# Kernel optimization log

Hardware: AMD Instinct MI355X
Metric: run time of the kernel (lower is better)

The kernel has to match this reference:

```python
import jax, jax.numpy as jnp
import numpy as np
import math

B, T, D = 4, 4096, 512
LN_EPS = 1e-5


def setup_inputs() -> dict:
    key = jax.random.key(0)
    ks = jax.random.split(key, 12)
    stdv = 1.0 / math.sqrt(D)
    lin = 1.0 / math.sqrt(D)  # torch Linear default init bound
    return {
        "query": jax.random.normal(ks[0], (B, T, D), jnp.float32),
        "value": jax.random.normal(ks[1], (B, T, D), jnp.float32),
        "query_vector": jax.random.uniform(ks[2], (D,), jnp.float32, -stdv, stdv),
        "key_vector": jax.random.uniform(ks[3], (D,), jnp.float32, -stdv, stdv),
        "value_vector": jax.random.uniform(ks[4], (D,), jnp.float32, -stdv, stdv),
        "Wq": jax.random.uniform(ks[5], (D, D), jnp.float32, -lin, lin),
        "bq": jax.random.uniform(ks[6], (D,), jnp.float32, -lin, lin),
        "ln_gamma": jnp.ones((D,), jnp.float32),
        "ln_beta": jnp.zeros((D,), jnp.float32),
        "Ws": jax.random.uniform(ks[7], (D, D), jnp.float32, -lin, lin),
        "bs": jax.random.uniform(ks[8], (D,), jnp.float32, -lin, lin),
        "Wt": jax.random.uniform(ks[9], (D, D), jnp.float32, -lin, lin),
        "bt": jax.random.uniform(ks[10], (D,), jnp.float32, -lin, lin),
    }


def reference(query, value, query_vector, key_vector, value_vector,
              Wq, bq, ln_gamma, ln_beta, Ws, bs, Wt, bt):
    d = query.shape[-1]
    # query linear + layernorm
    q = query @ Wq.T + bq
    mu = jnp.mean(q, axis=-1, keepdims=True)
    var = jnp.var(q, axis=-1, keepdims=True)
    q = (q - mu) * jax.lax.rsqrt(var + LN_EPS) * ln_gamma + ln_beta
    # gated Q/K/V preprocessing
    q = q * jax.nn.sigmoid(query_vector)
    k = value * jax.nn.sigmoid(key_vector)
    vv = jax.nn.sigmoid(value_vector)              # [D]
    v_sigm = jax.nn.sigmoid(vv @ Ws.T + bs)        # [D] (infer=False path)
    v_tanh = jnp.tanh(vv @ Wt.T + bt)              # [D]
    v = value * (v_sigm * v_tanh)
    # causal full attention (explicit, as in original)
    w = jnp.einsum('btd,bsd->bts', q, k) / jnp.sqrt(jnp.float32(d))
    tmask = jnp.tril(jnp.ones((q.shape[1], q.shape[1]), bool))
    w = jnp.where(tmask[None, :, :], w, -jnp.inf)
    w = jax.nn.softmax(w, axis=-1)
    return jnp.einsum('bts,bsd->btd', w, v)
```

## Files before the change

### kernel.cpp

```cpp
#include <hip/hip_runtime.h>
#include <cstdint>

typedef __bf16 bf16x8 __attribute__((ext_vector_type(8)));
typedef float f32x4 __attribute__((ext_vector_type(4)));

#define DIM 512
#define TSEQ 4096

__device__ __forceinline__ ushort f2bf(float x) {
  uint32_t u = __float_as_uint(x);
  u += 0x7fffu + ((u >> 16) & 1u);
  return (ushort)(u >> 16);
}
__device__ __forceinline__ float bf2f(ushort u) {
  return __uint_as_float(((uint32_t)u) << 16);
}

__global__ __launch_bounds__(512)
void gates_kernel(const float* __restrict__ qv, const float* __restrict__ kv,
                  const float* __restrict__ vvec,
                  const float* __restrict__ Ws, const float* __restrict__ bs,
                  const float* __restrict__ Wt, const float* __restrict__ bt,
                  const float* __restrict__ gamma, const float* __restrict__ beta,
                  float* __restrict__ gk, float* __restrict__ gv,
                  float* __restrict__ gb1, float* __restrict__ gb2) {
  __shared__ float vv[DIM];
  const int t = threadIdx.x;
  const int lane = t & 63, w = t >> 6;
  vv[t] = 1.f / (1.f + __expf(-vvec[t]));
  if (blockIdx.x == 0) {
    const float SC = 0.044194173824159216f;
    float gqv = 1.f / (1.f + __expf(-qv[t]));
    gk[t] = 1.f / (1.f + __expf(-kv[t]));
    gb1[t] = gamma[t] * gqv * SC;
    gb2[t] = beta[t] * gqv * SC;
  }
  __syncthreads();
  const int d = blockIdx.x * 8 + w;
  const float* wsr = Ws + (size_t)d * DIM + lane * 8;
  const float* wtr = Wt + (size_t)d * DIM + lane * 8;
  float4 v0 = *(const float4*)(&vv[lane * 8]);
  float4 v1 = *(const float4*)(&vv[lane * 8 + 4]);
  float4 s0 = *(const float4*)wsr, s1 = *(const float4*)(wsr + 4);
  float4 t0 = *(const float4*)wtr, t1 = *(const float4*)(wtr + 4);
  float as = v0.x*s0.x + v0.y*s0.y + v0.z*s0.z + v0.w*s0.w
           + v1.x*s1.x + v1.y*s1.y + v1.z*s1.z + v1.w*s1.w;
  float at = v0.x*t0.x + v0.y*t0.y + v0.z*t0.z + v0.w*t0.w
           + v1.x*t1.x + v1.y*t1.y + v1.z*t1.z + v1.w*t1.w;
  #pragma unroll
  for (int off = 1; off < 64; off <<= 1) {
    as += __shfl_xor(as, off, 64);
    at += __shfl_xor(at, off, 64);
  }
  if (lane == 0) {
    float sg = 1.f / (1.f + __expf(-(as + bs[d])));
    float th = tanhf(at + bt[d]);
    gv[d] = sg * th;
  }
}

__global__ __launch_bounds__(256)
void wconv_kernel(const float* __restrict__ W, ushort* __restrict__ Wb) {
  int i = blockIdx.x * 256 + threadIdx.x;
  float4 v = ((const float4*)W)[i];
  ushort4 o = { f2bf(v.x), f2bf(v.y), f2bf(v.z), f2bf(v.w) };
  ((ushort4*)Wb)[i] = o;
}

__global__ __launch_bounds__(256, 2)
void qgemmln_kernel(const float* __restrict__ A, const ushort* __restrict__ Wb,
                    const float* __restrict__ bq,
                    const float* __restrict__ gb1, const float* __restrict__ gb2,
                    ushort* __restrict__ qout) {
  __shared__ ushort As[32][40];
  __shared__ float rws[4][32], rws2[4][32];
  const int t = threadIdx.x;
  const int lane = t & 63, w = t >> 6;
  const int r16 = lane & 15, kb8 = lane >> 4;
  const int rowbase = blockIdx.x * 32;
  f32x4 acc[2][8];
  #pragma unroll
  for (int m = 0; m < 2; ++m)
    #pragma unroll
    for (int n = 0; n < 8; ++n) acc[m][n] = (f32x4)0.f;

  for (int kb = 0; kb < 16; ++kb) {
    const int k0 = kb * 32;
    __syncthreads();
    {
      int ar = t >> 3, ac = (t & 7) * 4;
      float4 a = *(const float4*)(A + (size_t)(rowbase + ar) * DIM + k0 + ac);
      ushort4 u = { f2bf(a.x), f2bf(a.y), f2bf(a.z), f2bf(a.w) };
      *(ushort4*)&As[ar][ac] = u;
    }
    __syncthreads();
    bf16x8 a0 = *(const bf16x8*)&As[r16][kb8 * 8];
    bf16x8 a1 = *(const bf16x8*)&As[16 + r16][kb8 * 8];
    #pragma unroll
    for (int n = 0; n < 8; ++n) {
      bf16x8 bb = *(const bf16x8*)(Wb + (size_t)(w * 128 + n * 16 + r16) * DIM + k0 + kb8 * 8);
      acc[0][n] = __builtin_amdgcn_mfma_f32_16x16x32_bf16(a0, bb, acc[0][n], 0, 0, 0);
      acc[1][n] = __builtin_amdgcn_mfma_f32_16x16x32_bf16(a1, bb, acc[1][n], 0, 0, 0);
    }
  }
  float s_[2][4], ss_[2][4];
  #pragma unroll
  for (int m = 0; m < 2; ++m)
    #pragma unroll
    for (int r = 0; r < 4; ++r) { s_[m][r] = 0.f; ss_[m][r] = 0.f; }
  #pragma unroll
  for (int n = 0; n < 8; ++n) {
    float bqv = bq[w * 128 + n * 16 + r16];
    #pragma unroll
    for (int m = 0; m < 2; ++m)
      #pragma unroll
      for (int r = 0; r < 4; ++r) {
        float v = acc[m][n][r] + bqv;
        acc[m][n][r] = v;
        s_[m][r] += v;
        ss_[m][r] += v * v;
      }
  }
  #pragma unroll
  for (int m = 0; m < 2; ++m)
    #pragma unroll
    for (int r = 0; r < 4; ++r)
      #pragma unroll
      for (int off = 1; off < 16; off <<= 1) {
        s_[m][r]  += __shfl_xor(s_[m][r], off, 64);
        ss_[m][r] += __shfl_xor(ss_[m][r], off, 64);
      }
  if (r16 == 0) {
    #pragma unroll
    for (int m = 0; m < 2; ++m)
      #pragma unroll
      for (int r = 0; r < 4; ++r) {
        int row = m * 16 + kb8 * 4 + r;
        rws[w][row]  = s_[m][r];
        rws2[w][row] = ss_[m][r];
      }
  }
  __syncthreads();
  float mu_[2][4], rs_[2][4];
  #pragma unroll
  for (int m = 0; m < 2; ++m)
    #pragma unroll
    for (int r = 0; r < 4; ++r) {
      int row = m * 16 + kb8 * 4 + r;
      float s = rws[0][row] + rws[1][row] + rws[2][row] + rws[3][row];
      float q = rws2[0][row] + rws2[1][row] + rws2[2][row] + rws2[3][row];
      float mu = s * (1.f / DIM);
      float var = q * (1.f / DIM) - mu * mu;
      mu_[m][r] = mu;
      rs_[m][r] = rsqrtf(var + 1e-5f);
    }
  #pragma unroll
  for (int n = 0; n < 8; ++n) {
    int col = w * 128 + n * 16 + r16;
    float g1 = gb1[col], g2 = gb2[col];
    #pragma unroll
    for (int m = 0; m < 2; ++m)
      #pragma unroll
      for (int r = 0; r < 4; ++r) {
        int row = rowbase + m * 16 + kb8 * 4 + r;
        float o = (acc[m][n][r] - mu_[m][r]) * rs_[m][r] * g1 + g2;
        qout[(size_t)row * DIM + col] = f2bf(o);
      }
  }
}

__global__ __launch_bounds__(256)
void vkprep_kernel(const float* __restrict__ value, const float* __restrict__ gk,
                   const float* __restrict__ gv,
                   ushort* __restrict__ kbuf, ushort* __restrict__ vT) {
  __shared__ ushort tile[64][73];
  const int t = threadIdx.x;
  const int s0 = blockIdx.x * 64, d0 = blockIdx.y * 64;
  const size_t boff = (size_t)blockIdx.z * TSEQ * DIM;
  #pragma unroll
  for (int rep = 0; rep < 4; ++rep) {
    int f = rep * 1024 + t * 4;
    int sr = f >> 6, dc = f & 63;
    float4 v = *(const float4*)(value + boff + (size_t)(s0 + sr) * DIM + d0 + dc);
    float4 g = *(const float4*)(gv + d0 + dc);
    float4 gg = *(const float4*)(gk + d0 + dc);
    tile[sr][dc]     = f2bf(v.x * g.x);
    tile[sr][dc + 1] = f2bf(v.y * g.y);
    tile[sr][dc + 2] = f2bf(v.z * g.z);
    tile[sr][dc + 3] = f2bf(v.w * g.w);
    ushort4 ko = { f2bf(v.x*gg.x), f2bf(v.y*gg.y), f2bf(v.z*gg.z), f2bf(v.w*gg.w) };
    *(ushort4*)(kbuf + boff + (size_t)(s0 + sr) * DIM + d0 + dc) = ko;
  }
  __syncthreads();
  const int d = t >> 2, sc0 = (t & 3) * 16;
  __align__(16) ushort tmp[16];
  #pragma unroll
  for (int j = 0; j < 16; ++j) tmp[j] = tile[sc0 + j][d];
  ushort* dst = vT + (size_t)blockIdx.z * DIM * TSEQ + (size_t)(d0 + d) * TSEQ + s0 + sc0;
  ((uint4*)dst)[0] = *(const uint4*)&tmp[0];
  ((uint4*)dst)[1] = *(const uint4*)&tmp[8];
}

__global__ __launch_bounds__(512)
void attn6_kernel(const ushort* __restrict__ qb, const ushort* __restrict__ kb,
                  const ushort* __restrict__ vT, float* __restrict__ out,
                  ushort* __restrict__ pO, float* __restrict__ stats) {
  __shared__ __align__(16) float Sp[4][64][68];
  __shared__ __align__(16) ushort P[64][72];
  __shared__ float lrow[64];

  const int t = threadIdx.x;
  const int lane = t & 63;
  const int w = t >> 6;
  const int r16 = lane & 15;
  const int kb8 = lane >> 4;
  const int dcQ = w & 3;
  const int h = w >> 2;

  const int bid = blockIdx.x;
  const int wg = ((bid & 7) << 5) | (bid >> 3);
  const int b = wg >> 6;
  const int rr = wg & 63;
  const int s = rr >> 1;
  const int half = rr & 1;

  const size_t boff  = (size_t)b * TSEQ * DIM;
  const size_t vboff = (size_t)b * DIM * TSEQ;

  for (int ji = 0; ji < 2; ++ji) {
    int qt, kt0, kt1, mode, cid;
    if (half) {
      if (ji) break;
      qt = 63 - s; kt0 = 31 - s; kt1 = 64 - s; mode = 1; cid = (b*32 + s)*2 + 1;
    } else if (ji == 0) {
      qt = s; kt0 = 0; kt1 = s + 1; mode = 0; cid = 0;
    } else {
      qt = 63 - s; kt0 = 0; kt1 = 31 - s; mode = 1; cid = (b*32 + s)*2;
    }
    const int qbase = qt * 64;

    __syncthreads();
    if (t < 64) lrow[t] = 0.f;
    bf16x8 aQ[4][4];
    #pragma unroll
    for (int m = 0; m < 4; ++m)
      #pragma unroll
      for (int c = 0; c < 4; ++c)
        aQ[m][c] = *(const bf16x8*)(qb + boff + (size_t)(qbase + m*16 + r16) * DIM
                                    + dcQ*128 + c*32 + kb8*8);
    f32x4 accO[4][4];
    #pragma unroll
    for (int m = 0; m < 4; ++m)
      #pragma unroll
      for (int n = 0; n < 4; ++n) accO[m][n] = (f32x4)0.f;

    {
      const int kbase = kt0 * 64;
      f32x4 accS[4][2];
      #pragma unroll
      for (int m = 0; m < 4; ++m) { accS[m][0] = (f32x4)0.f; accS[m][1] = (f32x4)0.f; }
      #pragma unroll
      for (int c = 0; c < 4; ++c) {
        bf16x8 bK0 = *(const bf16x8*)(kb + boff + (size_t)(kbase + h*32 + r16) * DIM
                                      + dcQ*128 + c*32 + kb8*8);
        bf16x8 bK1 = *(const bf16x8*)(kb + boff + (size_t)(kbase + h*32 + 16 + r16) * DIM
                                      + dcQ*128 + c*32 + kb8*8);
        #pragma unroll
        for (int m = 0; m < 4; ++m) {
          accS[m][0] = __builtin_amdgcn_mfma_f32_16x16x32_bf16(bK0, aQ[m][c], accS[m][0], 0, 0, 0);
          accS[m][1] = __builtin_amdgcn_mfma_f32_16x16x32_bf16(bK1, aQ[m][c], accS[m][1], 0, 0, 0);
        }
      }
      #pragma unroll
      for (int m = 0; m < 4; ++m)
        #pragma unroll
        for (int n = 0; n < 2; ++n)
          *(f32x4*)&Sp[dcQ][m*16 + r16][h*32 + n*16 + kb8*4] = accS[m][n];
    }
    __syncthreads();

    for (int kt = kt0; kt < kt1; ++kt) {
      const int kbase = kt * 64;
      const bool havek = (kt + 1 < kt1);

      bf16x8 kpre[8], vpre[8];
      if (havek) {
        const int kb2 = (kt + 1) * 64;
        #pragma unroll
        for (int c = 0; c < 4; ++c) {
          kpre[c*2]     = *(const bf16x8*)(kb + boff + (size_t)(kb2 + h*32 + r16) * DIM
                                           + dcQ*128 + c*32 + kb8*8);
          kpre[c*2 + 1] = *(const bf16x8*)(kb + boff + (size_t)(kb2 + h*32 + 16 + r16) * DIM
                                           + dcQ*128 + c*32 + kb8*8);
        }
      }
      #pragma unroll
      for (int n = 0; n < 4; ++n)
        #pragma unroll
        for (int c = 0; c < 2; ++c)
          vpre[n*2 + c] = *(const bf16x8*)(vT + vboff + (size_t)(w*64 + n*16 + r16) * TSEQ
                                           + kbase + c*32 + kb8*8);

      {
        const int row = t >> 3, c0 = (t & 7) * 8;
        float sv[8];
        #pragma unroll
        for (int j = 0; j < 8; ++j) sv[j] = 0.f;
        #pragma unroll
        for (int ch = 0; ch < 4; ++ch) {
          float4 u0 = *(const float4*)&Sp[ch][row][c0];
          float4 u1 = *(const float4*)&Sp[ch][row][c0 + 4];
          sv[0] += u0.x; sv[1] += u0.y; sv[2] += u0.z; sv[3] += u0.w;
          sv[4] += u1.x; sv[5] += u1.y; sv[6] += u1.z; sv[7] += u1.w;
        }
        const int qg = qbase + row;
        float ps = 0.f;
        #pragma unroll
        for (int j = 0; j < 8; ++j) {
          sv[j] = (kbase + c0 + j > qg) ? 0.f : __expf(sv[j]);
          ps += sv[j];
        }
        ps += __shfl_xor(ps, 1, 64);
        ps += __shfl_xor(ps, 2, 64);
        ps += __shfl_xor(ps, 4, 64);
        ushort4 p0 = { f2bf(sv[0]), f2bf(sv[1]), f2bf(sv[2]), f2bf(sv[3]) };
        ushort4 p1 = { f2bf(sv[4]), f2bf(sv[5]), f2bf(sv[6]), f2bf(sv[7]) };
        *(ushort4*)&P[row][c0] = p0;
        *(ushort4*)&P[row][c0 + 4] = p1;
        if ((t & 7) == 0) lrow[row] += ps;
      }
      __syncthreads();

      __builtin_amdgcn_s_setprio(1);
      #pragma unroll
      for (int c = 0; c < 2; ++c) {
        bf16x8 aP[4];
        #pragma unroll
        for (int m = 0; m < 4; ++m) aP[m] = *(const bf16x8*)&P[m*16 + r16][c*32 + kb8*8];
        #pragma unroll
        for (int n = 0; n < 4; ++n)
          #pragma unroll
          for (int m = 0; m < 4; ++m)
            accO[m][n] = __builtin_amdgcn_mfma_f32_16x16x32_bf16(aP[m], vpre[n*2 + c],
                                                                 accO[m][n], 0, 0, 0);
      }
      if (havek) {
        f32x4 accS[4][2];
        #pragma unroll
        for (int m = 0; m < 4; ++m) { accS[m][0] = (f32x4)0.f; accS[m][1] = (f32x4)0.f; }
        #pragma unroll
        for (int c = 0; c < 4; ++c)
          #pragma unroll
          for (int m = 0; m < 4; ++m) {
            accS[m][0] = __builtin_amdgcn_mfma_f32_16x16x32_bf16(kpre[c*2],     aQ[m][c], accS[m][0], 0, 0, 0);
            accS[m][1] = __builtin_amdgcn_mfma_f32_16x16x32_bf16(kpre[c*2 + 1], aQ[m][c], accS[m][1], 0, 0, 0);
          }
        #pragma unroll
        for (int m = 0; m < 4; ++m)
          #pragma unroll
          for (int n = 0; n < 2; ++n)
            *(f32x4*)&Sp[dcQ][m*16 + r16][h*32 + n*16 + kb8*4] = accS[m][n];
      }
      __builtin_amdgcn_s_setprio(0);
      __syncthreads();
    }

    if (mode == 0) {
      #pragma unroll
      for (int m = 0; m < 4; ++m)
        #pragma unroll
        for (int r = 0; r < 4; ++r) {
          int row = m*16 + kb8*4 + r;
          float inv = 1.f / lrow[row];
          float* dst = out + boff + (size_t)(qbase + row) * DIM + w*64 + r16;
          #pragma unroll
          for (int n = 0; n < 4; ++n) dst[n*16] = accO[m][n][r] * inv;
        }
    } else {
      ushort* po = pO + (size_t)cid * (64 * DIM);
      #pragma unroll
      for (int m = 0; m < 4; ++m)
        #pragma unroll
        for (int r = 0; r < 4; ++r) {
          int row = m*16 + kb8*4 + r;
          ushort* dst = po + (size_t)row * DIM + w*64 + r16;
          #pragma unroll
          for (int n = 0; n < 4; ++n) dst[n*16] = f2bf(accO[m][n][r]);
        }
      if (t < 64) stats[(size_t)cid*64 + t] = lrow[t];
    }
  }
}

__global__ __launch_bounds__(256)
void comb_kernel(const ushort* __restrict__ pO, const float* __restrict__ stats,
                 float* __restrict__ out) {
  const int g = blockIdx.x;
  const int rb = blockIdx.y;
  const int t = threadIdx.x;
  const int b = g >> 5, s = g & 31, qt = 63 - s;
  const int row = rb * 4 + (t >> 6);
  const int col = (t & 63) * 8;
  float l0 = stats[(size_t)(g*2 + 0)*64 + row];
  float l1 = stats[(size_t)(g*2 + 1)*64 + row];
  float inv = 1.f / (l0 + l1);
  const ushort* pa = pO + ((size_t)(g*2 + 0) * 64 + row) * DIM + col;
  const ushort* pb = pO + ((size_t)(g*2 + 1) * 64 + row) * DIM + col;
  ushort4 a0 = ((const ushort4*)pa)[0], a1 = ((const ushort4*)pa)[1];
  ushort4 b0 = ((const ushort4*)pb)[0], b1 = ((const ushort4*)pb)[1];
  float* dst = out + ((size_t)b * TSEQ + (size_t)qt * 64 + row) * DIM + col;
  float4 o0 = { (bf2f(a0.x) + bf2f(b0.x)) * inv, (bf2f(a0.y) + bf2f(b0.y)) * inv,
                (bf2f(a0.z) + bf2f(b0.z)) * inv, (bf2f(a0.w) + bf2f(b0.w)) * inv };
  float4 o1 = { (bf2f(a1.x) + bf2f(b1.x)) * inv, (bf2f(a1.y) + bf2f(b1.y)) * inv,
                (bf2f(a1.z) + bf2f(b1.z)) * inv, (bf2f(a1.w) + bf2f(b1.w)) * inv };
  ((float4*)dst)[0] = o0;
  ((float4*)dst)[1] = o1;
}

extern "C" void kernel_launch(void* const* d_in, const int* in_sizes, int n_in,
                              void* d_out, int out_size, void* d_ws, size_t ws_size,
                              hipStream_t stream) {
  const float* query = (const float*)d_in[0];
  const float* value = (const float*)d_in[1];
  const float* qv    = (const float*)d_in[2];
  const float* kv    = (const float*)d_in[3];
  const float* vvec  = (const float*)d_in[4];
  const float* Wq    = (const float*)d_in[5];
  const float* bq    = (const float*)d_in[6];
  const float* gam   = (const float*)d_in[7];
  const float* bet   = (const float*)d_in[8];
  const float* Ws    = (const float*)d_in[9];
  const float* bs    = (const float*)d_in[10];
  const float* Wt    = (const float*)d_in[11];
  const float* bt    = (const float*)d_in[12];
  float* out = (float*)d_out;

  char* ws = (char*)d_ws;
  float*  gk    = (float*)(ws);
  float*  gv    = (float*)(ws + 2048);
  float*  gb1   = (float*)(ws + 4096);
  float*  gb2   = (float*)(ws + 6144);
  ushort* Wb    = (ushort*)(ws + 8192);
  float*  stats = (float*)(ws + 532480);
  ushort* pO    = (ushort*)(ws + 663552);
  ushort* qb    = (ushort*)(ws + 17440768);
  ushort* kb    = (ushort*)(ws + 34217984);
  ushort* vT    = (ushort*)(ws + 50995200);

  gates_kernel<<<64, 512, 0, stream>>>(qv, kv, vvec, Ws, bs, Wt, bt, gam, bet,
                                       gk, gv, gb1, gb2);
  wconv_kernel<<<256, 256, 0, stream>>>(Wq, Wb);
  qgemmln_kernel<<<512, 256, 0, stream>>>(query, Wb, bq, gb1, gb2, qb);
  vkprep_kernel<<<dim3(64, 8, 4), 256, 0, stream>>>(value, gk, gv, kb, vT);
  attn6_kernel<<<256, 512, 0, stream>>>(qb, kb, vT, out, pO, stats);
  comb_kernel<<<dim3(128, 16), 256, 0, stream>>>(pO, stats, out);
}
```

Baseline: 224.4 us.

## Shrink attention query tile to 32 rows with 4-wave blocks and doubled grid

The attention kernel now processes 32-row query tiles with 256 threads, giving 512 blocks instead of 256. Each wave owns a 128-column slice of D, so the old K/V register prefetch goes away and V is loaded directly inside the PV loop. The causal work pairing and split/combine layout are reworked for 128 query tiles against 64-wide key tiles. The intent is better load balance and occupancy across CUs, at the cost of lower K/V reuse per block, more global loads, and less latency hiding.

```diff
diff --git a/kernel.cpp b/kernel.cpp
--- a/kernel.cpp
+++ b/kernel.cpp
@@ -201,105 +201,92 @@
   ((uint4*)dst)[1] = *(const uint4*)&tmp[8];
 }
 
-__global__ __launch_bounds__(512)
-void attn6_kernel(const ushort* __restrict__ qb, const ushort* __restrict__ kb,
+__global__ __launch_bounds__(256)
+void attn7_kernel(const ushort* __restrict__ qb, const ushort* __restrict__ kb,
                   const ushort* __restrict__ vT, float* __restrict__ out,
                   ushort* __restrict__ pO, float* __restrict__ stats) {
-  __shared__ __align__(16) float Sp[4][64][68];
-  __shared__ __align__(16) ushort P[64][72];
-  __shared__ float lrow[64];
+  __shared__ __align__(16) float Sp[4][32][68];
+  __shared__ __align__(16) ushort P[32][72];
+  __shared__ float lrow[32];
 
   const int t = threadIdx.x;
   const int lane = t & 63;
-  const int w = t >> 6;
+  const int dcQ = t >> 6;
   const int r16 = lane & 15;
   const int kb8 = lane >> 4;
-  const int dcQ = w & 3;
-  const int h = w >> 2;
 
   const int bid = blockIdx.x;
-  const int wg = ((bid & 7) << 5) | (bid >> 3);
-  const int b = wg >> 6;
-  const int rr = wg & 63;
-  const int s = rr >> 1;
-  const int half = rr & 1;
+  const int job = ((bid & 7) << 6) | (bid >> 3);
+  const int pid = job >> 1;
+  const int half = job & 1;
+  const int b = pid >> 6;
+  const int p = pid & 63;
 
   const size_t boff  = (size_t)b * TSEQ * DIM;
   const size_t vboff = (size_t)b * DIM * TSEQ;
+  const int nk_small = (p >> 1) + 1;
+  const int nk_large = ((127 - p) >> 1) + 1;
+  const int prefix = 32 - nk_small;
 
   for (int ji = 0; ji < 2; ++ji) {
     int qt, kt0, kt1, mode, cid;
     if (half) {
       if (ji) break;
-      qt = 63 - s; kt0 = 31 - s; kt1 = 64 - s; mode = 1; cid = (b*32 + s)*2 + 1;
+      qt = 127 - p; kt0 = prefix; kt1 = nk_large; mode = 1; cid = pid*2 + 1;
     } else if (ji == 0) {
-      qt = s; kt0 = 0; kt1 = s + 1; mode = 0; cid = 0;
+      qt = p; kt0 = 0; kt1 = nk_small; mode = 0; cid = 0;
     } else {
-      qt = 63 - s; kt0 = 0; kt1 = 31 - s; mode = 1; cid = (b*32 + s)*2;
-    }
-    const int qbase = qt * 64;
+      qt = 127 - p; kt0 = 0; kt1 = prefix; mode = 1; cid = pid*2;
+    }
+    const int qbase = qt * 32;
 
     __syncthreads();
-    if (t < 64) lrow[t] = 0.f;
-    bf16x8 aQ[4][4];
-    #pragma unroll
-    for (int m = 0; m < 4; ++m)
+    if (t < 32) lrow[t] = 0.f;
+
+    bf16x8 aQ[2][4];
+    #pragma unroll
+    for (int m = 0; m < 2; ++m)
       #pragma unroll
       for (int c = 0; c < 4; ++c)
         aQ[m][c] = *(const bf16x8*)(qb + boff + (size_t)(qbase + m*16 + r16) * DIM
                                     + dcQ*128 + c*32 + kb8*8);
-    f32x4 accO[4][4];
-    #pragma unroll
-    for (int m = 0; m < 4; ++m)
-      #pragma unroll
-      for (int n = 0; n < 4; ++n) accO[m][n] = (f32x4)0.f;
-
-    {
+    f32x4 accO[2][8];
+    #pragma unroll
+    for (int m = 0; m < 2; ++m)
+      #pragma unroll
+      for (int n = 0; n < 8; ++n) accO[m][n] = (f32x4)0.f;
+
+    if (kt0 < kt1) {
       const int kbase = kt0 * 64;
-      f32x4 accS[4][2];
-      #pragma unroll
-      for (int m = 0; m < 4; ++m) { accS[m][0] = (f32x4)0.f; accS[m][1] = (f32x4)0.f; }
+      f32x4 accS[2][4];
+      #pragma unroll
+      for (int m = 0; m < 2; ++m)
+        #pragma unroll
+        for (int n = 0; n < 4; ++n) accS[m][n] = (f32x4)0.f;
       #pragma unroll
       for (int c = 0; c < 4; ++c) {
-        bf16x8 bK0 = *(const bf16x8*)(kb + boff + (size_t)(kbase + h*32 + r16) * DIM
-                                      + dcQ*128 + c*32 + kb8*8);
-        bf16x8 bK1 = *(const bf16x8*)(kb + boff + (size_t)(kbase + h*32 + 16 + r16) * DIM
-                                      + dcQ*128 + c*32 + kb8*8);
-        #pragma unroll
-        for (int m = 0; m < 4; ++m) {
-          accS[m][0] = __builtin_amdgcn_mfma_f32_16x16x32_bf16(bK0, aQ[m][c], accS[m][0], 0, 0, 0);
-          accS[m][1] = __builtin_amdgcn_mfma_f32_16x16x32_bf16(bK1, aQ[m][c], accS[m][1], 0, 0, 0);
-        }
-      }
-      #pragma unroll
-      for (int m = 0; m < 4; ++m)
-        #pragma unroll
-        for (int n = 0; n < 2; ++n)
-          *(f32x4*)&Sp[dcQ][m*16 + r16][h*32 + n*16 + kb8*4] = accS[m][n];
+        bf16x8 bK[4];
+        #pragma unroll
+        for (int n = 0; n < 4; ++n)
+          bK[n] = *(const bf16x8*)(kb + boff + (size_t)(kbase + n*16 + r16) * DIM
+                                   + dcQ*128 + c*32 + kb8*8);
+        #pragma unroll
+        for (int m = 0; m < 2; ++m)
+          #pragma unroll
+          for (int n = 0; n < 4; ++n)
+            accS[m][n] = __builtin_amdgcn_mfma_f32_16x16x32_bf16(bK[n], aQ[m][c], accS[m][n], 0, 0, 0);
+      }
+      #pragma unroll
+      for (int m = 0; m < 2; ++m)
+        #pragma unroll
+        for (int n = 0; n < 4; ++n)
+          *(f32x4*)&Sp[dcQ][m*16 + r16][n*16 + kb8*4] = accS[m][n];
     }
     __syncthreads();
 
     for (int kt = kt0; kt < kt1; ++kt) {
       const int kbase = kt * 64;
       const bool havek = (kt + 1 < kt1);
-
-      bf16x8 kpre[8], vpre[8];
-      if (havek) {
-        const int kb2 = (kt + 1) * 64;
-        #pragma unroll
-        for (int c = 0; c < 4; ++c) {
-          kpre[c*2]     = *(const bf16x8*)(kb + boff + (size_t)(kb2 + h*32 + r16) * DIM
-                                           + dcQ*128 + c*32 + kb8*8);
-          kpre[c*2 + 1] = *(const bf16x8*)(kb + boff + (size_t)(kb2 + h*32 + 16 + r16) * DIM
-                                           + dcQ*128 + c*32 + kb8*8);
-        }
-      }
-      #pragma unroll
-      for (int n = 0; n < 4; ++n)
-        #pragma unroll
-        for (int c = 0; c < 2; ++c)
-          vpre[n*2 + c] = *(const bf16x8*)(vT + vboff + (size_t)(w*64 + n*16 + r16) * TSEQ
-                                           + kbase + c*32 + kb8*8);
 
       {
         const int row = t >> 3, c0 = (t & 7) * 8;
@@ -334,32 +321,42 @@
       __builtin_amdgcn_s_setprio(1);
       #pragma unroll
       for (int c = 0; c < 2; ++c) {
-        bf16x8 aP[4];
-        #pragma unroll
-        for (int m = 0; m < 4; ++m) aP[m] = *(const bf16x8*)&P[m*16 + r16][c*32 + kb8*8];
-        #pragma unroll
-        for (int n = 0; n < 4; ++n)
-          #pragma unroll
-          for (int m = 0; m < 4; ++m)
-            accO[m][n] = __builtin_amdgcn_mfma_f32_16x16x32_bf16(aP[m], vpre[n*2 + c],
-                                                                 accO[m][n], 0, 0, 0);
+        bf16x8 aP[2];
+        aP[0] = *(const bf16x8*)&P[r16][c*32 + kb8*8];
+        aP[1] = *(const bf16x8*)&P[16 + r16][c*32 + kb8*8];
+        #pragma unroll
+        for (int n = 0; n < 8; ++n) {
+          bf16x8 bV = *(const bf16x8*)(vT + vboff + (size_t)(dcQ*128 + n*16 + r16) * TSEQ
+                                       + kbase + c*32 + kb8*8);
+          accO[0][n] = __builtin_amdgcn_mfma_f32_16x16x32_bf16(aP[0], bV, accO[0][n], 0, 0, 0);
+          accO[1][n] = __builtin_amdgcn_mfma_f32_16x16x32_bf16(aP[1], bV, accO[1][n], 0, 0, 0);
+        }
       }
       if (havek) {
-        f32x4 accS[4][2];
-        #pragma unroll
-        for (int m = 0; m < 4; ++m) { accS[m][0] = (f32x4)0.f; accS[m][1] = (f32x4)0.f; }
-        #pragma unroll
-        for (int c = 0; c < 4; ++c)
-          #pragma unroll
-          for (int m = 0; m < 4; ++m) {
-            accS[m][0] = __builtin_amdgcn_mfma_f32_16x16x32_bf16(kpre[c*2],     aQ[m][c], accS[m][0], 0, 0, 0);
-            accS[m][1] = __builtin_amdgcn_mfma_f32_16x16x32_bf16(kpre[c*2 + 1], aQ[m][c], accS[m][1], 0, 0, 0);
-          }
-        #pragma unroll
-        for (int m = 0; m < 4; ++m)
-          #pragma unroll
-          for (int n = 0; n < 2; ++n)
-            *(f32x4*)&Sp[dcQ][m*16 + r16][h*32 + n*16 + kb8*4] = accS[m][n];
+        const int kb2 = (kt + 1) * 64;
+        f32x4 accS[2][4];
+        #pragma unroll
+        for (int m = 0; m < 2; ++m)
+          #pragma unroll
+          for (int n = 0; n < 4; ++n) accS[m][n] = (f32x4)0.f;
+        #pragma unroll
+        for (int c = 0; c < 4; ++c) {
+          bf16x8 bK[4];
+          #pragma unroll
+          for (int n = 0; n < 4; ++n)
+            bK[n] = *(const bf16x8*)(kb + boff + (size_t)(kb2 + n*16 + r16) * DIM
+                                     + dcQ*128 + c*32 + kb8*8);
+          #pragma unroll
+          for (int m = 0; m < 2; ++m)
+            #pragma unroll
+            for (int n = 0; n < 4; ++n)
+              accS[m][n] = __builtin_amdgcn_mfma_f32_16x16x32_bf16(bK[n], aQ[m][c], accS[m][n], 0, 0, 0);
+        }
+        #pragma unroll
+        for (int m = 0; m < 2; ++m)
+          #pragma unroll
+          for (int n = 0; n < 4; ++n)
+            *(f32x4*)&Sp[dcQ][m*16 + r16][n*16 + kb8*4] = accS[m][n];
       }
       __builtin_amdgcn_s_setprio(0);
       __syncthreads();
@@ -367,27 +364,27 @@
 
     if (mode == 0) {
       #pragma unroll
-      for (int m = 0; m < 4; ++m)
+      for (int m = 0; m < 2; ++m)
         #pragma unroll
         for (int r = 0; r < 4; ++r) {
           int row = m*16 + kb8*4 + r;
           float inv = 1.f / lrow[row];
-          float* dst = out + boff + (size_t)(qbase + row) * DIM + w*64 + r16;
-          #pragma unroll
-          for (int n = 0; n < 4; ++n) dst[n*16] = accO[m][n][r] * inv;
+          float* dst = out + boff + (size_t)(qbase + row) * DIM + dcQ*128 + r16;
+          #pragma unroll
+          for (int n = 0; n < 8; ++n) dst[n*16] = accO[m][n][r] * inv;
         }
     } else {
-      ushort* po = pO + (size_t)cid * (64 * DIM);
-      #pragma unroll
-      for (int m = 0; m < 4; ++m)
+      ushort* po = pO + (size_t)cid * (32 * DIM);
+      #pragma unroll
+      for (int m = 0; m < 2; ++m)
         #pragma unroll
         for (int r = 0; r < 4; ++r) {
           int row = m*16 + kb8*4 + r;
-          ushort* dst = po + (size_t)row * DIM + w*64 + r16;
-          #pragma unroll
-          for (int n = 0; n < 4; ++n) dst[n*16] = f2bf(accO[m][n][r]);
-        }
-      if (t < 64) stats[(size_t)cid*64 + t] = lrow[t];
+          ushort* dst = po + (size_t)row * DIM + dcQ*128 + r16;
+          #pragma unroll
+          for (int n = 0; n < 8; ++n) dst[n*16] = f2bf(accO[m][n][r]);
+        }
+      if (t < 32) stats[(size_t)cid*32 + t] = lrow[t];
     }
   }
 }
@@ -398,17 +395,17 @@
   const int g = blockIdx.x;
   const int rb = blockIdx.y;
   const int t = threadIdx.x;
-  const int b = g >> 5, s = g & 31, qt = 63 - s;
+  const int b = g >> 6, p = g & 63, qt = 127 - p;
   const int row = rb * 4 + (t >> 6);
   const int col = (t & 63) * 8;
-  float l0 = stats[(size_t)(g*2 + 0)*64 + row];
-  float l1 = stats[(size_t)(g*2 + 1)*64 + row];
+  float l0 = stats[(size_t)(g*2 + 0)*32 + row];
+  float l1 = stats[(size_t)(g*2 + 1)*32 + row];
   float inv = 1.f / (l0 + l1);
-  const ushort* pa = pO + ((size_t)(g*2 + 0) * 64 + row) * DIM + col;
-  const ushort* pb = pO + ((size_t)(g*2 + 1) * 64 + row) * DIM + col;
+  const ushort* pa = pO + ((size_t)(g*2 + 0) * 32 + row) * DIM + col;
+  const ushort* pb = pO + ((size_t)(g*2 + 1) * 32 + row) * DIM + col;
   ushort4 a0 = ((const ushort4*)pa)[0], a1 = ((const ushort4*)pa)[1];
   ushort4 b0 = ((const ushort4*)pb)[0], b1 = ((const ushort4*)pb)[1];
-  float* dst = out + ((size_t)b * TSEQ + (size_t)qt * 64 + row) * DIM + col;
+  float* dst = out + ((size_t)b * TSEQ + (size_t)qt * 32 + row) * DIM + col;
   float4 o0 = { (bf2f(a0.x) + bf2f(b0.x)) * inv, (bf2f(a0.y) + bf2f(b0.y)) * inv,
                 (bf2f(a0.z) + bf2f(b0.z)) * inv, (bf2f(a0.w) + bf2f(b0.w)) * inv };
   float4 o1 = { (bf2f(a1.x) + bf2f(b1.x)) * inv, (bf2f(a1.y) + bf2f(b1.y)) * inv,
@@ -452,6 +449,6 @@
   wconv_kernel<<<256, 256, 0, stream>>>(Wq, Wb);
   qgemmln_kernel<<<512, 256, 0, stream>>>(query, Wb, bq, gb1, gb2, qb);
   vkprep_kernel<<<dim3(64, 8, 4), 256, 0, stream>>>(value, gk, gv, kb, vT);
-  attn6_kernel<<<256, 512, 0, stream>>>(qb, kb, vT, out, pO, stats);
-  comb_kernel<<<dim3(128, 16), 256, 0, stream>>>(pO, stats, out);
-}
+  attn7_kernel<<<512, 256, 0, stream>>>(qb, kb, vT, out, pO, stats);
+  comb_kernel<<<dim3(256, 8), 256, 0, stream>>>(pO, stats, out);
+}
```

Measured after the change: 366.8 us. +63.5%, slower.

## Restructure attention into double-buffered ping-pong pipeline with new wave split

Applied to the files above, without the earlier changes.

Replaces the attention kernel with one that double-buffers the score and probability tiles in shared memory, so the QK^T of one key tile, the softmax of another and the PV of a third run within a single barrier interval. The wave decomposition changes from 4 d-chunks by 2 key halves to 2 d-chunks by 2 key halves by 2 query halves. Each wave now owns a 32x128 output slice, and V is loaded directly inside the PV step instead of being prefetched. It also requests 2 blocks per CU through launch bounds, which raises register pressure risk. An unused attn8_kernel variant is left in the file.

```diff
diff --git a/kernel.cpp b/kernel.cpp
--- a/kernel.cpp
+++ b/kernel.cpp
@@ -11,9 +11,6 @@
   uint32_t u = __float_as_uint(x);
   u += 0x7fffu + ((u >> 16) & 1u);
   return (ushort)(u >> 16);
-}
-__device__ __forceinline__ float bf2f(ushort u) {
-  return __uint_as_float(((uint32_t)u) << 16);
 }
 
 __global__ __launch_bounds__(512)
@@ -201,12 +198,11 @@
   ((uint4*)dst)[1] = *(const uint4*)&tmp[8];
 }
 
-__global__ __launch_bounds__(512)
-void attn6_kernel(const ushort* __restrict__ qb, const ushort* __restrict__ kb,
-                  const ushort* __restrict__ vT, float* __restrict__ out,
-                  ushort* __restrict__ pO, float* __restrict__ stats) {
-  __shared__ __align__(16) float Sp[4][64][68];
-  __shared__ __align__(16) ushort P[64][72];
+__global__ __launch_bounds__(512, 2)
+void attn8_kernel(const ushort* __restrict__ qb, const ushort* __restrict__ kb,
+                  const ushort* __restrict__ vT, float* __restrict__ out) {
+  __shared__ __align__(16) float Sp[2][2][64][68];
+  __shared__ __align__(16) ushort P[2][64][72];
   __shared__ float lrow[64];
 
   const int t = threadIdx.x;
@@ -214,178 +210,333 @@
   const int w = t >> 6;
   const int r16 = lane & 15;
   const int kb8 = lane >> 4;
-  const int dcQ = w & 3;
-  const int h = w >> 2;
+  const int dc = w & 1;
+  const int h  = (w >> 1) & 1;
+  const int qh = w >> 2;
+  const int dcol = (w & 3) * 128;
 
   const int bid = blockIdx.x;
   const int wg = ((bid & 7) << 5) | (bid >> 3);
   const int b = wg >> 6;
-  const int rr = wg & 63;
-  const int s = rr >> 1;
-  const int half = rr & 1;
+  const int s = (wg & 63);
+  const int sp = s >> 1;
+  const int ph = s & 1;
+  (void)sp; (void)ph;
+  const int u = wg & 63;
+  const int s2 = u >> 1;
+  const int half = u & 1;
 
   const size_t boff  = (size_t)b * TSEQ * DIM;
   const size_t vboff = (size_t)b * DIM * TSEQ;
+
+  int qbase = 0;
+
+  bf16x8 aQ[2][8];
+  f32x4 accO[2][8];
+
+  auto qkt = [&](int st, int kt) {
+    const int kbase = kt * 64;
+    f32x4 accS[2][2];
+    #pragma unroll
+    for (int m = 0; m < 2; ++m) { accS[m][0] = (f32x4)0.f; accS[m][1] = (f32x4)0.f; }
+    #pragma unroll
+    for (int c = 0; c < 8; ++c) {
+      bf16x8 bK0 = *(const bf16x8*)(kb + boff + (size_t)(kbase + h*32 + r16) * DIM
+                                    + dc*256 + c*32 + kb8*8);
+      bf16x8 bK1 = *(const bf16x8*)(kb + boff + (size_t)(kbase + h*32 + 16 + r16) * DIM
+                                    + dc*256 + c*32 + kb8*8);
+      #pragma unroll
+      for (int m = 0; m < 2; ++m) {
+        accS[m][0] = __builtin_amdgcn_mfma_f32_16x16x32_bf16(bK0, aQ[m][c], accS[m][0], 0, 0, 0);
+        accS[m][1] = __builtin_amdgcn_mfma_f32_16x16x32_bf16(bK1, aQ[m][c], accS[m][1], 0, 0, 0);
+      }
+    }
+    #pragma unroll
+    for (int m = 0; m < 2; ++m)
+      #pragma unroll
+      for (int n = 0; n < 2; ++n)
+        *(f32x4*)&Sp[st][dc][qh*32 + m*16 + r16][h*32 + n*16 + kb8*4] = accS[m][n];
+  };
+
+  auto sm = [&](int st, int kt) {
+    const int kbase = kt * 64;
+    const int row = t >> 3, c0 = (t & 7) * 8;
+    float4 u0 = *(const float4*)&Sp[st][0][row][c0];
+    float4 u1 = *(const float4*)&Sp[st][0][row][c0 + 4];
+    float4 w0 = *(const float4*)&Sp[st][1][row][c0];
+    float4 w1 = *(const float4*)&Sp[st][1][row][c0 + 4];
+    float sv[8] = { u0.x + w0.x, u0.y + w0.y, u0.z + w0.z, u0.w + w0.w,
+                    u1.x + w1.x, u1.y + w1.y, u1.z + w1.z, u1.w + w1.w };
+    const int qg = qbase + row;
+    float ps = 0.f;
+    #pragma unroll
+    for (int j = 0; j < 8; ++j) {
+      sv[j] = (kbase + c0 + j > qg) ? 0.f : __expf(sv[j]);
+      ps += sv[j];
+    }
+    ps += __shfl_xor(ps, 1, 64);
+    ps += __shfl_xor(ps, 2, 64);
+    ps += __shfl_xor(ps, 4, 64);
+    __align__(16) ushort tmp[8];
+    #pragma unroll
+    for (int j = 0; j < 8; ++j) tmp[j] = f2bf(sv[j]);
+    *(uint4*)&P[st][row][c0] = *(const uint4*)tmp;
+    if ((t & 7) == 0) lrow[row] += ps;
+  };
+
+  auto pv = [&](int st, int kt) {
+    const int kbase = kt * 64;
+    #pragma unroll
+    for (int c = 0; c < 2; ++c) {
+      bf16x8 aP0 = *(const bf16x8*)&P[st][qh*32 + r16][c*32 + kb8*8];
+      bf16x8 aP1 = *(const bf16x8*)&P[st][qh*32 + 16 + r16][c*32 + kb8*8];
+      #pragma unroll
+      for (int n = 0; n < 8; ++n) {
+        bf16x8 bV = *(const bf16x8*)(vT + vboff + (size_t)(dcol + n*16 + r16) * TSEQ
+                                     + kbase + c*32 + kb8*8);
+        accO[0][n] = __builtin_amdgcn_mfma_f32_16x16x32_bf16(aP0, bV, accO[0][n], 0, 0, 0);
+        accO[1][n] = __builtin_amdgcn_mfma_f32_16x16x32_bf16(aP1, bV, accO[1][n], 0, 0, 0);
+      }
+    }
+  };
 
   for (int ji = 0; ji < 2; ++ji) {
     int qt, kt0, kt1, mode, cid;
     if (half) {
       if (ji) break;
-      qt = 63 - s; kt0 = 31 - s; kt1 = 64 - s; mode = 1; cid = (b*32 + s)*2 + 1;
+      qt = 63 - s2; kt0 = 31 - s2; kt1 = 64 - s2; mode = 1; cid = (b*32 + s2)*2 + 1;
     } else if (ji == 0) {
-      qt = s; kt0 = 0; kt1 = s + 1; mode = 0; cid = 0;
+      qt = s2; kt0 = 0; kt1 = s2 + 1; mode = 0; cid = 0;
     } else {
-      qt = 63 - s; kt0 = 0; kt1 = 31 - s; mode = 1; cid = (b*32 + s)*2;
-    }
-    const int qbase = qt * 64;
+      qt = 63 - s2; kt0 = 0; kt1 = 31 - s2; mode = 1; cid = (b*32 + s2)*2;
+    }
+    qbase = qt * 64;
+    const int N = kt1 - kt0;
 
     __syncthreads();
     if (t < 64) lrow[t] = 0.f;
-    bf16x8 aQ[4][4];
-    #pragma unroll
-    for (int m = 0; m < 4; ++m)
-      #pragma unroll
-      for (int c = 0; c < 4; ++c)
-        aQ[m][c] = *(const bf16x8*)(qb + boff + (size_t)(qbase + m*16 + r16) * DIM
-                                    + dcQ*128 + c*32 + kb8*8);
-    f32x4 accO[4][4];
-    #pragma unroll
-    for (int m = 0; m < 4; ++m)
-      #pragma unroll
-      for (int n = 0; n < 4; ++n) accO[m][n] = (f32x4)0.f;
-
-    {
-      const int kbase = kt0 * 64;
-      f32x4 accS[4][2];
-      #pragma unroll
-      for (int m = 0; m < 4; ++m) { accS[m][0] = (f32x4)0.f; accS[m][1] = (f32x4)0.f; }
-      #pragma unroll
-      for (int c = 0; c < 4; ++c) {
-        bf16x8 bK0 = *(const bf16x8*)(kb + boff + (size_t)(kbase + h*32 + r16) * DIM
-                                      + dcQ*128 + c*32 + kb8*8);
-        bf16x8 bK1 = *(const bf16x8*)(kb + boff + (size_t)(kbase + h*32 + 16 + r16) * DIM
-                                      + dcQ*128 + c*32 + kb8*8);
-        #pragma unroll
-        for (int m = 0; m < 4; ++m) {
-          accS[m][0] = __builtin_amdgcn_mfma_f32_16x16x32_bf16(bK0, aQ[m][c], accS[m][0], 0, 0, 0);
-          accS[m][1] = __builtin_amdgcn_mfma_f32_16x16x32_bf16(bK1, aQ[m][c], accS[m][1], 0, 0, 0);
-        }
-      }
-      #pragma unroll
-      for (int m = 0; m < 4; ++m)
-        #pragma unroll
-        for (int n = 0; n < 2; ++n)
-          *(f32x4*)&Sp[dcQ][m*16 + r16][h*32 + n*16 + kb8*4] = accS[m][n];
-    }
-    __syncthreads();
-
-    for (int kt = kt0; kt < kt1; ++kt) {
-      const int kbase = kt * 64;
-      const bool havek = (kt + 1 < kt1);
-
-      bf16x8 kpre[8], vpre[8];
-      if (havek) {
-        const int kb2 = (kt + 1) * 64;
-        #pragma unroll
-        for (int c = 0; c < 4; ++c) {
-          kpre[c*2]     = *(const bf16x8*)(kb + boff + (size_t)(kb2 + h*32 + r16) * DIM
-                                           + dcQ*128 + c*32 + kb8*8);
-          kpre[c*2 + 1] = *(const bf16x8*)(kb + boff + (size_t)(kb2 + h*32 + 16 + r16) * DIM
-                                           + dcQ*128 + c*32 + kb8*8);
-        }
-      }
-      #pragma unroll
-      for (int n = 0; n < 4; ++n)
-        #pragma unroll
-        for (int c = 0; c < 2; ++c)
-          vpre[n*2 + c] = *(const bf16x8*)(vT + vboff + (size_t)(w*64 + n*16 + r16) * TSEQ
-                                           + kbase + c*32 + kb8*8);
-
-      {
-        const int row = t >> 3, c0 = (t & 7) * 8;
-        float sv[8];
-        #pragma unroll
-        for (int j = 0; j < 8; ++j) sv[j] = 0.f;
-        #pragma unroll
-        for (int ch = 0; ch < 4; ++ch) {
-          float4 u0 = *(const float4*)&Sp[ch][row][c0];
-          float4 u1 = *(const float4*)&Sp[ch][row][c0 + 4];
-          sv[0] += u0.x; sv[1] += u0.y; sv[2] += u0.z; sv[3] += u0.w;
-          sv[4] += u1.x; sv[5] += u1.y; sv[6] += u1.z; sv[7] += u1.w;
-        }
-        const int qg = qbase + row;
-        float ps = 0.f;
-        #pragma unroll
-        for (int j = 0; j < 8; ++j) {
-          sv[j] = (kbase + c0 + j > qg) ? 0.f : __expf(sv[j]);
-          ps += sv[j];
-        }
-        ps += __shfl_xor(ps, 1, 64);
-        ps += __shfl_xor(ps, 2, 64);
-        ps += __shfl_xor(ps, 4, 64);
-        ushort4 p0 = { f2bf(sv[0]), f2bf(sv[1]), f2bf(sv[2]), f2bf(sv[3]) };
-        ushort4 p1 = { f2bf(sv[4]), f2bf(sv[5]), f2bf(sv[6]), f2bf(sv[7]) };
-        *(ushort4*)&P[row][c0] = p0;
-        *(ushort4*)&P[row][c0 + 4] = p1;
-        if ((t & 7) == 0) lrow[row] += ps;
-      }
-      __syncthreads();
-
+    #pragma unroll
+    for (int m = 0; m < 2; ++m)
+      #pragma unroll
+      for (int c = 0; c < 8; ++c)
+        aQ[m][c] = *(const bf16x8*)(qb + boff + (size_t)(qbase + qh*32 + m*16 + r16) * DIM
+                                    + dc*256 + c*32 + kb8*8);
+    #pragma unroll
+    for (int m = 0; m < 2; ++m)
+      #pragma unroll
+      for (int n = 0; n < 8; ++n) accO[m][n] = (f32x4)0.f;
+
+    const int nA = (N + 1) >> 1, nB = N >> 1;
+
+    qkt(0, kt0);
+    __syncthreads();
+    sm(0, kt0);
+    if (nB > 0) qkt(1, kt0 + 1);
+    __syncthreads();
+
+    for (int p = 0; p < nA; ++p) {
       __builtin_amdgcn_s_setprio(1);
-      #pragma unroll
-      for (int c = 0; c < 2; ++c) {
-        bf16x8 aP[4];
-        #pragma unroll
-        for (int m = 0; m < 4; ++m) aP[m] = *(const bf16x8*)&P[m*16 + r16][c*32 + kb8*8];
-        #pragma unroll
-        for (int n = 0; n < 4; ++n)
-          #pragma unroll
-          for (int m = 0; m < 4; ++m)
-            accO[m][n] = __builtin_amdgcn_mfma_f32_16x16x32_bf16(aP[m], vpre[n*2 + c],
-                                                                 accO[m][n], 0, 0, 0);
-      }
-      if (havek) {
-        f32x4 accS[4][2];
-        #pragma unroll
-        for (int m = 0; m < 4; ++m) { accS[m][0] = (f32x4)0.f; accS[m][1] = (f32x4)0.f; }
-        #pragma unroll
-        for (int c = 0; c < 4; ++c)
-          #pragma unroll
-          for (int m = 0; m < 4; ++m) {
-            accS[m][0] = __builtin_amdgcn_mfma_f32_16x16x32_bf16(kpre[c*2],     aQ[m][c], accS[m][0], 0, 0, 0);
-            accS[m][1] = __builtin_amdgcn_mfma_f32_16x16x32_bf16(kpre[c*2 + 1], aQ[m][c], accS[m][1], 0, 0, 0);
-          }
-        #pragma unroll
-        for (int m = 0; m < 4; ++m)
-          #pragma unroll
-          for (int n = 0; n < 2; ++n)
-            *(f32x4*)&Sp[dcQ][m*16 + r16][h*32 + n*16 + kb8*4] = accS[m][n];
-      }
+      pv(0, kt0 + 2*p);
+      if (p + 1 < nA) qkt(0, kt0 + 2*p + 2);
+      if (p < nB) sm(1, kt0 + 2*p + 1);
       __builtin_amdgcn_s_setprio(0);
       __syncthreads();
+      __builtin_amdgcn_s_setprio(1);
+      if (p < nB) pv(1, kt0 + 2*p + 1);
+      if (p + 1 < nB) qkt(1, kt0 + 2*p + 3);
+      if (p + 1 < nA) sm(0, kt0 + 2*p + 2);
+      __builtin_amdgcn_s_setprio(0);
+      __syncthreads();
     }
 
     if (mode == 0) {
       #pragma unroll
-      for (int m = 0; m < 4; ++m)
+      for (int m = 0; m < 2; ++m)
         #pragma unroll
         for (int r = 0; r < 4; ++r) {
-          int row = m*16 + kb8*4 + r;
-          float inv = 1.f / lrow[row];
-          float* dst = out + boff + (size_t)(qbase + row) * DIM + w*64 + r16;
+          int qrow = qh*32 + m*16 + kb8*4 + r;
+          float inv = 1.f / lrow[qrow];
+          float* dst = out + boff + (size_t)(qbase + qrow) * DIM + dcol + r16;
           #pragma unroll
-          for (int n = 0; n < 4; ++n) dst[n*16] = accO[m][n][r] * inv;
+          for (int n = 0; n < 8; ++n) dst[n*16] = accO[m][n][r] * inv;
+        }
+    } else {
+      float* po = (float*)out;
+      (void)po;
+    }
+    if (mode == 1) {
+    }
+  }
+}
+
+__global__ __launch_bounds__(512, 2)
+void attn8p_kernel(const ushort* __restrict__ qb, const ushort* __restrict__ kb,
+                   const ushort* __restrict__ vT, float* __restrict__ out,
+                   ushort* __restrict__ pO, float* __restrict__ stats) {
+  __shared__ __align__(16) float Sp[2][2][64][68];
+  __shared__ __align__(16) ushort P[2][64][72];
+  __shared__ float lrow[64];
+
+  const int t = threadIdx.x;
+  const int lane = t & 63;
+  const int w = t >> 6;
+  const int r16 = lane & 15;
+  const int kb8 = lane >> 4;
+  const int dc = w & 1;
+  const int h  = (w >> 1) & 1;
+  const int qh = w >> 2;
+  const int dcol = (w & 3) * 128;
+
+  const int bid = blockIdx.x;
+  const int wg = ((bid & 7) << 5) | (bid >> 3);
+  const int b = wg >> 6;
+  const int u = wg & 63;
+  const int s2 = u >> 1;
+  const int half = u & 1;
+
+  const size_t boff  = (size_t)b * TSEQ * DIM;
+  const size_t vboff = (size_t)b * DIM * TSEQ;
+
+  int qbase = 0;
+  bf16x8 aQ[2][8];
+  f32x4 accO[2][8];
+
+  auto qkt = [&](int st, int kt) {
+    const int kbase = kt * 64;
+    f32x4 accS[2][2];
+    #pragma unroll
+    for (int m = 0; m < 2; ++m) { accS[m][0] = (f32x4)0.f; accS[m][1] = (f32x4)0.f; }
+    #pragma unroll
+    for (int c = 0; c < 8; ++c) {
+      bf16x8 bK0 = *(const bf16x8*)(kb + boff + (size_t)(kbase + h*32 + r16) * DIM
+                                    + dc*256 + c*32 + kb8*8);
+      bf16x8 bK1 = *(const bf16x8*)(kb + boff + (size_t)(kbase + h*32 + 16 + r16) * DIM
+                                    + dc*256 + c*32 + kb8*8);
+      #pragma unroll
+      for (int m = 0; m < 2; ++m) {
+        accS[m][0] = __builtin_amdgcn_mfma_f32_16x16x32_bf16(bK0, aQ[m][c], accS[m][0], 0, 0, 0);
+        accS[m][1] = __builtin_amdgcn_mfma_f32_16x16x32_bf16(bK1, aQ[m][c], accS[m][1], 0, 0, 0);
+      }
+    }
+    #pragma unroll
+    for (int m = 0; m < 2; ++m)
+      #pragma unroll
+      for (int n = 0; n < 2; ++n)
+        *(f32x4*)&Sp[st][dc][qh*32 + m*16 + r16][h*32 + n*16 + kb8*4] = accS[m][n];
+  };
+
+  auto sm = [&](int st, int kt) {
+    const int kbase = kt * 64;
+    const int row = t >> 3, c0 = (t & 7) * 8;
+    float4 u0 = *(const float4*)&Sp[st][0][row][c0];
+    float4 u1 = *(const float4*)&Sp[st][0][row][c0 + 4];
+    float4 w0 = *(const float4*)&Sp[st][1][row][c0];
+    float4 w1 = *(const float4*)&Sp[st][1][row][c0 + 4];
+    float sv[8] = { u0.x + w0.x, u0.y + w0.y, u0.z + w0.z, u0.w + w0.w,
+                    u1.x + w1.x, u1.y + w1.y, u1.z + w1.z, u1.w + w1.w };
+    const int qg = qbase + row;
+    float ps = 0.f;
+    #pragma unroll
+    for (int j = 0; j < 8; ++j) {
+      sv[j] = (kbase + c0 + j > qg) ? 0.f : __expf(sv[j]);
+      ps += sv[j];
+    }
+    ps += __shfl_xor(ps, 1, 64);
+    ps += __shfl_xor(ps, 2, 64);
+    ps += __shfl_xor(ps, 4, 64);
+    __align__(16) ushort tmp[8];
+    #pragma unroll
+    for (int j = 0; j < 8; ++j) tmp[j] = f2bf(sv[j]);
+    *(uint4*)&P[st][row][c0] = *(const uint4*)tmp;
+    if ((t & 7) == 0) lrow[row] += ps;
+  };
+
+  auto pv = [&](int st, int kt) {
+    const int kbase = kt * 64;
+    #pragma unroll
+    for (int c = 0; c < 2; ++c) {
+      bf16x8 aP0 = *(const bf16x8*)&P[st][qh*32 + r16][c*32 + kb8*8];
+      bf16x8 aP1 = *(const bf16x8*)&P[st][qh*32 + 16 + r16][c*32 + kb8*8];
+      #pragma unroll
+      for (int n = 0; n < 8; ++n) {
+        bf16x8 bV = *(const bf16x8*)(vT + vboff + (size_t)(dcol + n*16 + r16) * TSEQ
+                                     + kbase + c*32 + kb8*8);
+        accO[0][n] = __builtin_amdgcn_mfma_f32_16x16x32_bf16(aP0, bV, accO[0][n], 0, 0, 0);
+        accO[1][n] = __builtin_amdgcn_mfma_f32_16x16x32_bf16(aP1, bV, accO[1][n], 0, 0, 0);
+      }
+    }
+  };
+
+  for (int ji = 0; ji < 2; ++ji) {
+    int qt, kt0, kt1, mode, cid;
+    if (half) {
+      if (ji) break;
+      qt = 63 - s2; kt0 = 31 - s2; kt1 = 64 - s2; mode = 1; cid = (b*32 + s2)*2 + 1;
+    } else if (ji == 0) {
+      qt = s2; kt0 = 0; kt1 = s2 + 1; mode = 0; cid = 0;
+    } else {
+      qt = 63 - s2; kt0 = 0; kt1 = 31 - s2; mode = 1; cid = (b*32 + s2)*2;
+    }
+    qbase = qt * 64;
+    const int N = kt1 - kt0;
+
+    __syncthreads();
+    if (t < 64) lrow[t] = 0.f;
+    #pragma unroll
+    for (int m = 0; m < 2; ++m)
+      #pragma unroll
+      for (int c = 0; c < 8; ++c)
+        aQ[m][c] = *(const bf16x8*)(qb + boff + (size_t)(qbase + qh*32 + m*16 + r16) * DIM
+                                    + dc*256 + c*32 + kb8*8);
+    #pragma unroll
+    for (int m = 0; m < 2; ++m)
+      #pragma unroll
+      for (int n = 0; n < 8; ++n) accO[m][n] = (f32x4)0.f;
+
+    const int nA = (N + 1) >> 1, nB = N >> 1;
+
+    qkt(0, kt0);
+    __syncthreads();
+    sm(0, kt0);
+    if (nB > 0) qkt(1, kt0 + 1);
+    __syncthreads();
+
+    for (int p = 0; p < nA; ++p) {
+      __builtin_amdgcn_s_setprio(1);
+      pv(0, kt0 + 2*p);
+      if (p + 1 < nA) qkt(0, kt0 + 2*p + 2);
+      if (p < nB) sm(1, kt0 + 2*p + 1);
+      __builtin_amdgcn_s_setprio(0);
+      __syncthreads();
+      __builtin_amdgcn_s_setprio(1);
+      if (p < nB) pv(1, kt0 + 2*p + 1);
+      if (p + 1 < nB) qkt(1, kt0 + 2*p + 3);
+      if (p + 1 < nA) sm(0, kt0 + 2*p + 2);
+      __builtin_amdgcn_s_setprio(0);
+      __syncthreads();
+    }
+
+    if (mode == 0) {
+      #pragma unroll
+      for (int m = 0; m < 2; ++m)
+        #pragma unroll
+        for (int r = 0; r < 4; ++r) {
+          int qrow = qh*32 + m*16 + kb8*4 + r;
+          float inv = 1.f / lrow[qrow];
+          float* dst = out + boff + (size_t)(qbase + qrow) * DIM + dcol + r16;
+          #pragma unroll
+          for (int n = 0; n < 8; ++n) dst[n*16] = accO[m][n][r] * inv;
         }
     } else {
       ushort* po = pO + (size_t)cid * (64 * DIM);
       #pragma unroll
-      for (int m = 0; m < 4; ++m)
+      for (int m = 0; m < 2; ++m)
         #pragma unroll
         for (int r = 0; r < 4; ++r) {
-          int row = m*16 + kb8*4 + r;
-          ushort* dst = po + (size_t)row * DIM + w*64 + r16;
+          int qrow = qh*32 + m*16 + kb8*4 + r;
+          ushort* dst = po + (size_t)qrow * DIM + dcol + r16;
           #pragma unroll
-          for (int n = 0; n < 4; ++n) dst[n*16] = f2bf(accO[m][n][r]);
+          for (int n = 0; n < 8; ++n) dst[n*16] = f2bf(accO[m][n][r]);
         }
       if (t < 64) stats[(size_t)cid*64 + t] = lrow[t];
     }
@@ -408,6 +559,7 @@
   const ushort* pb = pO + ((size_t)(g*2 + 1) * 64 + row) * DIM + col;
   ushort4 a0 = ((const ushort4*)pa)[0], a1 = ((const ushort4*)pa)[1];
   ushort4 b0 = ((const ushort4*)pb)[0], b1 = ((const ushort4*)pb)[1];
+  auto bf2f = [](ushort uu) { return __uint_as_float(((uint32_t)uu) << 16); };
   float* dst = out + ((size_t)b * TSEQ + (size_t)qt * 64 + row) * DIM + col;
   float4 o0 = { (bf2f(a0.x) + bf2f(b0.x)) * inv, (bf2f(a0.y) + bf2f(b0.y)) * inv,
                 (bf2f(a0.z) + bf2f(b0.z)) * inv, (bf2f(a0.w) + bf2f(b0.w)) * inv };
@@ -452,6 +604,6 @@
   wconv_kernel<<<256, 256, 0, stream>>>(Wq, Wb);
   qgemmln_kernel<<<512, 256, 0, stream>>>(query, Wb, bq, gb1, gb2, qb);
   vkprep_kernel<<<dim3(64, 8, 4), 256, 0, stream>>>(value, gk, gv, kb, vT);
-  attn6_kernel<<<256, 512, 0, stream>>>(qb, kb, vT, out, pO, stats);
+  attn8p_kernel<<<256, 512, 0, stream>>>(qb, kb, vT, out, pO, stats);
   comb_kernel<<<dim3(128, 16), 256, 0, stream>>>(pO, stats, out);
 }
```

New measurement: 333.8 us. 48.7% more time.
